# Kernel tuning notes

Hardware: AMD Instinct MI355X
Metric: run time of the kernel (lower is better)

## Reference

```python
import jax, jax.numpy as jnp
import numpy as np

NEG_INF = -1e30

def dwconv1(x, dw, db, pw, pb):
    # DWConv with kernel_size=1: depthwise = per-channel scale+bias, pointwise = dense linear.
    # x: [B, L, H]
    return (x * dw + db) @ pw.T + pb

def masked_softmax(logits, maskf, axis):
    # masked_softmax as in SQuAD repos: mask*logits + (1-mask)*(-1e30), then softmax over axis
    m = maskf * logits + (1.0 - maskf) * NEG_INF
    return jax.nn.softmax(m, axis=axis)

def setup_inputs() -> dict:
    key = jax.random.key(0)
    ks = jax.random.split(key, 20)
    B, L, H = 4, 4096, 1024
    s = 1.0 / np.sqrt(H)
    inp = {
        "x": jax.random.normal(ks[0], (B, L, H), dtype=jnp.float32),
        "mask": jax.random.randint(ks[1], (B, L), 0, 2, dtype=jnp.int32),
    }
    names = ["k", "q", "v", "r"]
    for i, n in enumerate(names):
        inp[n + "_dw"] = jax.random.normal(ks[2 + 4 * i], (H,), dtype=jnp.float32) * 0.1 + 1.0
        inp[n + "_db"] = jnp.zeros((H,), dtype=jnp.float32)
        inp[n + "_pw"] = jax.random.normal(ks[3 + 4 * i], (H, H), dtype=jnp.float32) * s
        inp[n + "_pb"] = jnp.zeros((H,), dtype=jnp.float32)
    return inp

def reference(x, mask, k_dw, k_db, k_pw, k_pb, q_dw, q_db, q_pw, q_pb,
              v_dw, v_db, v_pw, v_pb, r_dw, r_db, r_pw, r_pb):
    B, L, H = x.shape
    n_head = 16
    hc = H // n_head
    maskf = mask.astype(x.dtype)[:, None, None, :]  # [B,1,1,L]

    def heads(t):  # [B,L,H] -> [B,nh,hc,L]
        return t.reshape(B, L, n_head, hc).transpose(0, 2, 3, 1)

    keys = heads(dwconv1(x, k_dw, k_db, k_pw, k_pb))
    queries = heads(dwconv1(x, q_dw, q_db, q_pw, q_pb))
    values = heads(dwconv1(x, v_dw, v_db, v_pw, v_pb))

    key_sm = masked_softmax(keys, maskf, axis=3)      # softmax over L
    query_sm = masked_softmax(queries, maskf, axis=2)  # softmax over head channels

    # context = key @ value^T : [B,nh,hc,hc]
    context = jnp.einsum("bhcl,bhdl->bhcd", key_sm, values)
    # attended = context^T @ query : [B,nh,hc(value),L]
    attended = jnp.einsum("bhcd,bhcl->bhdl", context, query_sm)

    agg = attended.transpose(0, 3, 1, 2).reshape(B, L, H)  # concat heads, [B,L,H]
    # dropout is identity in eval mode
    return dwconv1(agg, r_dw, r_db, r_pw, r_pb)
```

## Files before the change

### kernel.cpp

```cpp
#include <hip/hip_runtime.h>
#include <stdint.h>

#define H 1024
#define LSEQ 4096
#define NBATCH 4
#define MT (NBATCH*LSEQ)

typedef __attribute__((ext_vector_type(8))) short bf16x8;
typedef __attribute__((ext_vector_type(4))) short s16x4;
typedef __attribute__((ext_vector_type(4))) float f32x4;

static __device__ __forceinline__ unsigned short f2bf(float f){
  union { float f; unsigned u; } v; v.f = f;
  unsigned u = v.u;
  return (unsigned short)((u + 0x7FFFu + ((u >> 16) & 1u)) >> 16);
}
static __device__ __forceinline__ float bf2f(unsigned short h){
  union { unsigned u; float f; } v; v.u = ((unsigned)h) << 16;
  return v.f;
}
static __device__ __forceinline__ void g2l16(const void* g, void* l){
  __builtin_amdgcn_global_load_lds((const __attribute__((address_space(1))) void*)g,
                                   (__attribute__((address_space(3))) void*)l, 16, 0, 0);
}
static __device__ __forceinline__ f32x4 mfma16(bf16x8 a, bf16x8 b, f32x4 c){
  return __builtin_amdgcn_mfma_f32_16x16x32_bf16(a, b, c, 0, 0, 0);
}

struct P4 { const float* pw[4]; const float* dw[4]; const float* db[4]; const float* pb[4]; };

__global__ __launch_bounds__(256) void prep_w(P4 a, short* __restrict__ wb, float* __restrict__ bo){
  __shared__ float red[256];
  const int g = blockIdx.x, p = g >> 10, j = g & 1023, t = threadIdx.x;
  const float* row = a.pw[p] + (size_t)j * H;
  const float* dwp = a.dw[p];
  const float* dbp = a.db[p];
  float acc = 0.f;
  #pragma unroll
  for (int k = 0; k < 4; ++k){
    int i = k*256 + t;
    float pv = row[i];
    wb[((size_t)p*H + j)*H + i] = (short)f2bf(pv * dwp[i]);
    acc += dbp[i] * pv;
  }
  red[t] = acc; __syncthreads();
  for (int s = 128; s > 0; s >>= 1){
    if (t < s) red[t] += red[t+s];
    __syncthreads();
  }
  if (t == 0) bo[p*H + j] = a.pb[p][j] + red[0];
}

__global__ __launch_bounds__(256) void cvt_x(const float* __restrict__ x, short* __restrict__ xb){
  int i = blockIdx.x*256 + threadIdx.x;
  const float4* p = (const float4*)(x + (size_t)i*8);
  float4 a = p[0], b = p[1];
  bf16x8 o;
  o[0]=(short)f2bf(a.x); o[1]=(short)f2bf(a.y); o[2]=(short)f2bf(a.z); o[3]=(short)f2bf(a.w);
  o[4]=(short)f2bf(b.x); o[5]=(short)f2bf(b.y); o[6]=(short)f2bf(b.z); o[7]=(short)f2bf(b.w);
  *(bf16x8*)(xb + (size_t)i*8) = o;
}

template<int MODE, int NBLK>
__global__ __launch_bounds__(512, 2) void gemm8(const short* __restrict__ A,
    const short* __restrict__ WBp, const float* __restrict__ bia,
    short* __restrict__ oq, short* __restrict__ okT, short* __restrict__ ovT,
    float* __restrict__ ofin){
  __shared__ __align__(16) short lA[2][256*64];
  __shared__ __align__(16) short lB[2][256*64];

  const int nwg = NBLK * 64;
  const int cpx = nwg >> 3;
  const int bid = blockIdx.x;
  const int swz = (bid & 7) * cpx + (bid >> 3);
  const int mb = swz / NBLK, nb = swz % NBLK;
  const int m0 = mb * 256, n0 = nb * 256;

  const int tid  = threadIdx.x;
  const int lane = tid & 63;
  const int w    = tid >> 6;
  const int wm   = w >> 2, wn = w & 3;
  const int q4 = lane >> 4, r16 = lane & 15;
  const int rl = lane >> 3, sl = lane & 7;
  const int srcsw = ((sl ^ rl) << 3);

#define STAGE_A(BUF_, Q_, KB_) \
  g2l16(A + (size_t)(m0 + (Q_)*64 + w*8 + rl)*H + (KB_) + srcsw, \
        &lA[BUF_][((Q_)*64 + w*8)*64])
#define STAGE_B(BUF_, Q_, KB_) \
  g2l16(WBp + (size_t)(n0 + (Q_)*64 + w*8 + rl)*H + (KB_) + srcsw, \
        &lB[BUF_][((Q_)*64 + w*8)*64])
#define RD_A(dst, BUF_, MI8, KK) { const int row_ = wm*128 + (MI8)*16 + r16; \
  dst = *(const bf16x8*)&lA[BUF_][row_*64 + ((((KK)*4+q4) ^ (row_&7))<<3)]; }
#define RD_B(dst, BUF_, NI4, KK) { const int row_ = wn*64 + (NI4)*16 + r16; \
  dst = *(const bf16x8*)&lB[BUF_][row_*64 + ((((KK)*4+q4) ^ (row_&7))<<3)]; }

  f32x4 acc[8][4] = {};
  bf16x8 aF[4][2], bFa[2][2], bFb[2][2];

  STAGE_B(0,0,0); STAGE_B(0,1,0); STAGE_B(0,2,0); STAGE_B(0,3,0);
  STAGE_A(0,0,0); STAGE_A(0,2,0); STAGE_A(0,1,0); STAGE_A(0,3,0);
  asm volatile("s_waitcnt vmcnt(2)" ::: "memory");
  __builtin_amdgcn_s_barrier();
  __builtin_amdgcn_sched_barrier(0);

  #pragma unroll 2
  for (int t = 0; t < 16; ++t){
    const int buf = t & 1, sbuf = buf ^ 1;
    const int skb = ((t < 15) ? (t + 1) : 15) << 6;

    #pragma unroll
    for (int mi = 0; mi < 4; ++mi){ RD_A(aF[mi][0], buf, mi, 0); RD_A(aF[mi][1], buf, mi, 1); }
    #pragma unroll
    for (int ni = 0; ni < 2; ++ni){ RD_B(bFa[ni][0], buf, ni, 0); RD_B(bFa[ni][1], buf, ni, 1); }
    STAGE_B(sbuf, 0, skb); STAGE_B(sbuf, 1, skb);
    __builtin_amdgcn_s_barrier();
    asm volatile("s_waitcnt lgkmcnt(0)" ::: "memory");
    __builtin_amdgcn_sched_barrier(0);
    __builtin_amdgcn_s_setprio(1);
    #pragma unroll
    for (int kk = 0; kk < 2; ++kk)
      #pragma unroll
      for (int mi = 0; mi < 4; ++mi)
        #pragma unroll
        for (int ni = 0; ni < 2; ++ni)
          acc[mi][ni] = mfma16(aF[mi][kk], bFa[ni][kk], acc[mi][ni]);
    __builtin_amdgcn_s_setprio(0);
    __builtin_amdgcn_s_barrier();
    __builtin_amdgcn_sched_barrier(0);

    #pragma unroll
    for (int ni = 0; ni < 2; ++ni){ RD_B(bFb[ni][0], buf, 2+ni, 0); RD_B(bFb[ni][1], buf, 2+ni, 1); }
    STAGE_B(sbuf, 2, skb); STAGE_B(sbuf, 3, skb);
    __builtin_amdgcn_s_barrier();
    asm volatile("s_waitcnt lgkmcnt(0)" ::: "memory");
    __builtin_amdgcn_sched_barrier(0);
    __builtin_amdgcn_s_setprio(1);
    #pragma unroll
    for (int kk = 0; kk < 2; ++kk)
      #pragma unroll
      for (int mi = 0; mi < 4; ++mi)
        #pragma unroll
        for (int ni = 0; ni < 2; ++ni)
          acc[mi][2+ni] = mfma16(aF[mi][kk], bFb[ni][kk], acc[mi][2+ni]);
    __builtin_amdgcn_s_setprio(0);
    asm volatile("s_waitcnt vmcnt(4)" ::: "memory");
    __builtin_amdgcn_s_barrier();
    __builtin_amdgcn_sched_barrier(0);

    #pragma unroll
    for (int mi = 0; mi < 4; ++mi){ RD_A(aF[mi][0], buf, 4+mi, 0); RD_A(aF[mi][1], buf, 4+mi, 1); }
    STAGE_A(sbuf, 0, skb); STAGE_A(sbuf, 2, skb);
    __builtin_amdgcn_s_barrier();
    asm volatile("s_waitcnt lgkmcnt(0)" ::: "memory");
    __builtin_amdgcn_sched_barrier(0);
    __builtin_amdgcn_s_setprio(1);
    #pragma unroll
    for (int kk = 0; kk < 2; ++kk)
      #pragma unroll
      for (int mi = 0; mi < 4; ++mi)
        #pragma unroll
        for (int ni = 0; ni < 2; ++ni)
          acc[4+mi][ni] = mfma16(aF[mi][kk], bFa[ni][kk], acc[4+mi][ni]);
    __builtin_amdgcn_s_setprio(0);
    __builtin_amdgcn_s_barrier();
    __builtin_amdgcn_sched_barrier(0);

    STAGE_A(sbuf, 1, skb); STAGE_A(sbuf, 3, skb);
    __builtin_amdgcn_s_barrier();
    asm volatile("s_waitcnt lgkmcnt(0)" ::: "memory");
    __builtin_amdgcn_sched_barrier(0);
    __builtin_amdgcn_s_setprio(1);
    #pragma unroll
    for (int kk = 0; kk < 2; ++kk)
      #pragma unroll
      for (int mi = 0; mi < 4; ++mi)
        #pragma unroll
        for (int ni = 0; ni < 2; ++ni)
          acc[4+mi][2+ni] = mfma16(aF[mi][kk], bFb[ni][kk], acc[4+mi][2+ni]);
    __builtin_amdgcn_s_setprio(0);
    asm volatile("s_waitcnt vmcnt(2)" ::: "memory");
    __builtin_amdgcn_s_barrier();
    __builtin_amdgcn_sched_barrier(0);
  }
#undef STAGE_A
#undef STAGE_B
#undef RD_A
#undef RD_B

  if (MODE == 1){
    #pragma unroll
    for (int ni4 = 0; ni4 < 4; ++ni4){
      const int n = n0 + wn*64 + ni4*16 + r16;
      const float bv = bia[n];
      #pragma unroll
      for (int mi8 = 0; mi8 < 8; ++mi8){
        const int mbse = m0 + wm*128 + mi8*16 + q4*4;
        #pragma unroll
        for (int j = 0; j < 4; ++j)
          ofin[(size_t)(mbse+j)*H + n] = acc[mi8][ni4][j] + bv;
      }
    }
  } else {
    const int p = n0 >> 10;
    if (p == 1){
      #pragma unroll
      for (int ni4 = 0; ni4 < 4; ++ni4){
        const int n = n0 + wn*64 + ni4*16 + r16;
        const float bv = bia[n];
        const int ch = n & 1023;
        #pragma unroll
        for (int mi8 = 0; mi8 < 8; ++mi8){
          const int mbse = m0 + wm*128 + mi8*16 + q4*4;
          #pragma unroll
          for (int j = 0; j < 4; ++j)
            oq[(size_t)(mbse+j)*H + ch] = (short)f2bf(acc[mi8][ni4][j] + bv);
        }
      }
    } else {
      short* ot = (p == 0) ? okT : ovT;
      #pragma unroll
      for (int ni4 = 0; ni4 < 4; ++ni4){
        const int n = n0 + wn*64 + ni4*16 + r16;
        const float bv = bia[n];
        const int ch = n & 1023;
        #pragma unroll
        for (int mi8 = 0; mi8 < 8; ++mi8){
          const int m = m0 + wm*128 + mi8*16 + q4*4;
          const int bb = m >> 12, lpos = m & 4095;
          s16x4 v;
          #pragma unroll
          for (int j = 0; j < 4; ++j) v[j] = (short)f2bf(acc[mi8][ni4][j] + bv);
          *(s16x4*)&ot[((size_t)bb*H + ch)*LSEQ + lpos] = v;
        }
      }
    }
  }
}

__global__ __launch_bounds__(256) void key_stats(const short* __restrict__ kT,
    const int* __restrict__ mask, float* __restrict__ mx, float* __restrict__ rd){
  const int w = threadIdx.x >> 6, lane = threadIdx.x & 63;
  const int ch = blockIdx.x*4 + w;
  const int b = ch >> 10;
  const short* row = kT + (size_t)ch * LSEQ;
  const int* mrow = mask + (size_t)b * LSEQ;
  float vals[64];
  float m = -3e38f;
  #pragma unroll
  for (int it = 0; it < 8; ++it){
    const int l = it*512 + lane*8;
    bf16x8 v = *(const bf16x8*)&row[l];
    int4 k0 = *(const int4*)&mrow[l];
    int4 k1 = *(const int4*)&mrow[l+4];
    int mk[8] = {k0.x,k0.y,k0.z,k0.w,k1.x,k1.y,k1.z,k1.w};
    #pragma unroll
    for (int e=0;e<8;++e){
      float lg = mk[e] ? bf2f((unsigned short)v[e]) : -1e30f;
      vals[it*8+e] = lg;
      m = fmaxf(m, lg);
    }
  }
  #pragma unroll
  for (int off=32; off>=1; off>>=1) m = fmaxf(m, __shfl_xor(m, off));
  float s = 0.f;
  #pragma unroll
  for (int i=0;i<64;++i) s += __expf(vals[i]-m);
  #pragma unroll
  for (int off=32; off>=1; off>>=1) s += __shfl_xor(s, off);
  if (lane == 0){ mx[ch] = m; rd[ch] = 1.0f / s; }
}

__global__ __launch_bounds__(256) void ctx_k(const short* __restrict__ kT,
    const short* __restrict__ vT, const int* __restrict__ mask,
    const float* __restrict__ mx, const float* __restrict__ rd,
    float* __restrict__ ctxP){
  const int lc = blockIdx.x, h = blockIdx.y, b = blockIdx.z;
  __shared__ __align__(16) short lK[64*64];
  __shared__ __align__(16) short lV[64*64];
  __shared__ float sMx[64], sRd[64];
  __shared__ int sMk[64];
  const int tid = threadIdx.x, lane = tid & 63, w = tid >> 6;
  if (tid < 64){
    const int ch = b*1024 + h*64 + tid;
    sMx[tid] = mx[ch]; sRd[tid] = rd[ch];
  }
  f32x4 acc[4] = {};
  const short* kb = kT + (size_t)(b*16 + h)*64*LSEQ;
  const short* vb = vT + (size_t)(b*16 + h)*64*LSEQ;
  const int l0 = lc*1024;
  const int sl = lane & 7, rl = lane >> 3;
  const int lsw = ((sl ^ rl) << 3);
  for (int kc = 0; kc < 16; ++kc){
    __syncthreads();
    const int lb = l0 + kc*64;
    #pragma unroll
    for (int c = 0; c < 2; ++c){
      const int r = (w*2+c)*8 + rl;
      g2l16(kb + (size_t)r*LSEQ + lb + lsw, &lK[(w*2+c)*512]);
      g2l16(vb + (size_t)r*LSEQ + lb + lsw, &lV[(w*2+c)*512]);
    }
    if (tid < 64) sMk[tid] = mask[(size_t)b*LSEQ + lb + tid];
    __syncthreads();
    {
      const int row = lane;
      const float mxr = sMx[row], rdr = sRd[row];
      #pragma unroll
      for (int k2 = 0; k2 < 2; ++k2){
        const int slog = w*2 + k2;
        const int sp = slog ^ (row & 7);
        bf16x8 v = *(bf16x8*)&lK[row*64 + (sp<<3)];
        bf16x8 o;
        #pragma unroll
        for (int e=0;e<8;++e){
          const float f = bf2f((unsigned short)v[e]);
          const float lg = sMk[slog*8+e] ? f : -1e30f;
          o[e] = (short)f2bf(__expf(lg - mxr) * rdr);
        }
        *(bf16x8*)&lK[row*64 + (sp<<3)] = o;
      }
    }
    __syncthreads();
    const int q4 = lane >> 4, r16 = lane & 15;
    #pragma unroll
    for (int kk = 0; kk < 2; ++kk){
      const int slog = kk*4 + q4;
      const int rowA = w*16 + r16;
      bf16x8 a = *(bf16x8*)&lK[rowA*64 + ((slog ^ (rowA & 7))<<3)];
      #pragma unroll
      for (int ni = 0; ni < 4; ++ni){
        const int rowB = ni*16 + r16;
        bf16x8 bv = *(bf16x8*)&lV[rowB*64 + ((slog ^ (rowB & 7))<<3)];
        acc[ni] = mfma16(a, bv, acc[ni]);
      }
    }
  }
  const int q4 = lane >> 4, r16 = lane & 15;
  float* op = ctxP + (((size_t)(b*16 + h)*4 + lc) << 12);
  #pragma unroll
  for (int ni=0;ni<4;++ni){
    const int d = ni*16 + r16;
    #pragma unroll
    for (int j=0;j<4;++j){
      const int c = w*16 + q4*4 + j;
      op[c*64 + d] = acc[ni][j];
    }
  }
}

__global__ __launch_bounds__(256) void attd_k(const short* __restrict__ qb,
    const float* __restrict__ ctxP, const int* __restrict__ mask,
    short* __restrict__ agg){
  const int lcb = blockIdx.x, h = blockIdx.y, b = blockIdx.z;
  __shared__ __align__(16) short lQ[64*64];
  __shared__ __align__(16) short lCt[64*64];
  const int tid = threadIdx.x, lane = tid & 63, w = tid >> 6;
  {
    const int d = lane, g = w;
    const float* base = ctxP + ((size_t)(b*16 + h)*4 << 12);
    #pragma unroll
    for (int i=0;i<16;++i){
      const int c = g*16 + i;
      const float s = base[c*64+d] + base[4096+c*64+d] + base[8192+c*64+d] + base[12288+c*64+d];
      lCt[d*64 + ((((c>>3) ^ (d&7))<<3) | (c&7))] = (short)f2bf(s);
    }
  }
  const int l0g = b*LSEQ + lcb*1024;
  const int sl = lane & 7, rl = lane >> 3;
  const int lsw = ((sl ^ rl) << 3);
  for (int sc = 0; sc < 16; ++sc){
    __syncthreads();
    #pragma unroll
    for (int c = 0; c < 2; ++c){
      const int r = (w*2+c)*8 + rl;
      g2l16(qb + (size_t)(l0g + sc*64 + r)*H + h*64 + lsw, &lQ[(w*2+c)*512]);
    }
    __syncthreads();
    {
      const int row = w*16 + (lane & 15);
      const int q4 = lane >> 4;
      const int mk = mask[(size_t)b*LSEQ + lcb*1024 + sc*64 + row];
      float vals[16];
      float mxv = -3e38f;
      #pragma unroll
      for (int k2=0;k2<2;++k2){
        const int slog = q4*2 + k2;
        const int sp = slog ^ (row & 7);
        bf16x8 v = *(bf16x8*)&lQ[row*64 + (sp<<3)];
        #pragma unroll
        for (int e=0;e<8;++e){
          const float f = bf2f((unsigned short)v[e]);
          vals[k2*8+e] = f;
          mxv = fmaxf(mxv, f);
        }
      }
      mxv = fmaxf(mxv, __shfl_xor(mxv, 16));
      mxv = fmaxf(mxv, __shfl_xor(mxv, 32));
      float s = 0.f;
      #pragma unroll
      for (int e=0;e<16;++e){ vals[e] = __expf(vals[e]-mxv); s += vals[e]; }
      s += __shfl_xor(s, 16);
      s += __shfl_xor(s, 32);
      const float inv = 1.0f / s;
      #pragma unroll
      for (int k2=0;k2<2;++k2){
        const int slog = q4*2 + k2;
        const int sp = slog ^ (row & 7);
        bf16x8 o;
        #pragma unroll
        for (int e=0;e<8;++e)
          o[e] = (short)f2bf(mk ? vals[k2*8+e]*inv : 0.015625f);
        *(bf16x8*)&lQ[row*64 + (sp<<3)] = o;
      }
    }
    __syncthreads();
    f32x4 acc[4] = {};
    const int q4 = lane >> 4, r16 = lane & 15;
    #pragma unroll
    for (int kk=0;kk<2;++kk){
      const int slog = kk*4 + q4;
      const int rowA = w*16 + r16;
      bf16x8 a = *(bf16x8*)&lQ[rowA*64 + ((slog ^ (rowA&7))<<3)];
      #pragma unroll
      for (int ni=0;ni<4;++ni){
        const int rowB = ni*16 + r16;
        bf16x8 bv = *(bf16x8*)&lCt[rowB*64 + ((slog ^ (rowB&7))<<3)];
        acc[ni] = mfma16(a, bv, acc[ni]);
      }
    }
    #pragma unroll
    for (int ni=0;ni<4;++ni){
      const int d = ni*16 + r16;
      #pragma unroll
      for (int j=0;j<4;++j){
        const int lrow = w*16 + q4*4 + j;
        agg[(size_t)(l0g + sc*64 + lrow)*H + h*64 + d] = (short)f2bf(acc[ni][j]);
      }
    }
  }
}

extern "C" void kernel_launch(void* const* d_in, const int* in_sizes, int n_in,
                              void* d_out, int out_size, void* d_ws, size_t ws_size,
                              hipStream_t stream){
  (void)in_sizes; (void)n_in; (void)out_size; (void)ws_size;
  const float* x    = (const float*)d_in[0];
  const int*   mask = (const int*)d_in[1];
  P4 prm;
  for (int p2 = 0; p2 < 4; ++p2){
    prm.dw[p2] = (const float*)d_in[2 + 4*p2];
    prm.db[p2] = (const float*)d_in[3 + 4*p2];
    prm.pw[p2] = (const float*)d_in[4 + 4*p2];
    prm.pb[p2] = (const float*)d_in[5 + 4*p2];
  }
  char* ws = (char*)d_ws;
  short* WB   = (short*)(ws);
  float* BIAS = (float*)(ws + ((size_t)8<<20));
  float* MX   = BIAS + 4096;
  float* RD   = MX + 4096;
  short* XB   = (short*)(ws + ((size_t)9<<20));
  short* QB   = (short*)(ws + ((size_t)41<<20));
  short* KT   = (short*)(ws + ((size_t)73<<20));
  short* VT   = (short*)(ws + ((size_t)105<<20));
  float* CTXP = (float*)(ws + ((size_t)137<<20));
  short* AGG  = XB;

  prep_w<<<4096, 256, 0, stream>>>(prm, WB, BIAS);
  cvt_x<<<8192, 256, 0, stream>>>(x, XB);
  gemm8<0,12><<<768, 512, 0, stream>>>(XB, WB, BIAS, QB, KT, VT, nullptr);
  key_stats<<<1024, 256, 0, stream>>>(KT, mask, MX, RD);
  ctx_k<<<dim3(4,16,4), 256, 0, stream>>>(KT, VT, mask, MX, RD, CTXP);
  attd_k<<<dim3(4,16,4), 256, 0, stream>>>(QB, CTXP, mask, AGG);
  gemm8<1,4><<<256, 512, 0, stream>>>(AGG, WB + (size_t)3*H*H, BIAS + 3*1024,
                                      nullptr, nullptr, nullptr, (float*)d_out);
}
```

Baseline: 239.6 us.

## Merge GEMM MFMA phases and stage transposed K/V epilogue through LDS

Loads all four B fragments up front and merges each pair of MFMA phases into one, cutting the number of barriers per K iteration from eight to four. The transposed K/V epilogue now writes bf16 results into a swizzled LDS tile and reads them back as 16-byte rows, so global stores along L are fully coalesced instead of scattered 8-byte writes. A single LDS array replaces the separate A/B buffers so the epilogue can reuse it. This adds register pressure from holding more B fragments, plus two extra syncs in the epilogue.

```diff
diff --git a/kernel.cpp b/kernel.cpp
--- a/kernel.cpp
+++ b/kernel.cpp
@@ -66,8 +66,7 @@
     const short* __restrict__ WBp, const float* __restrict__ bia,
     short* __restrict__ oq, short* __restrict__ okT, short* __restrict__ ovT,
     float* __restrict__ ofin){
-  __shared__ __align__(16) short lA[2][256*64];
-  __shared__ __align__(16) short lB[2][256*64];
+  __shared__ __align__(16) short lsm[2][2][256*64];
 
   const int nwg = NBLK * 64;
   const int cpx = nwg >> 3;
@@ -86,14 +85,14 @@
 
 #define STAGE_A(BUF_, Q_, KB_) \
   g2l16(A + (size_t)(m0 + (Q_)*64 + w*8 + rl)*H + (KB_) + srcsw, \
-        &lA[BUF_][((Q_)*64 + w*8)*64])
+        &lsm[0][BUF_][((Q_)*64 + w*8)*64])
 #define STAGE_B(BUF_, Q_, KB_) \
   g2l16(WBp + (size_t)(n0 + (Q_)*64 + w*8 + rl)*H + (KB_) + srcsw, \
-        &lB[BUF_][((Q_)*64 + w*8)*64])
+        &lsm[1][BUF_][((Q_)*64 + w*8)*64])
 #define RD_A(dst, BUF_, MI8, KK) { const int row_ = wm*128 + (MI8)*16 + r16; \
-  dst = *(const bf16x8*)&lA[BUF_][row_*64 + ((((KK)*4+q4) ^ (row_&7))<<3)]; }
+  dst = *(const bf16x8*)&lsm[0][BUF_][row_*64 + ((((KK)*4+q4) ^ (row_&7))<<3)]; }
 #define RD_B(dst, BUF_, NI4, KK) { const int row_ = wn*64 + (NI4)*16 + r16; \
-  dst = *(const bf16x8*)&lB[BUF_][row_*64 + ((((KK)*4+q4) ^ (row_&7))<<3)]; }
+  dst = *(const bf16x8*)&lsm[1][BUF_][row_*64 + ((((KK)*4+q4) ^ (row_&7))<<3)]; }
 
   f32x4 acc[8][4] = {};
   bf16x8 aF[4][2], bFa[2][2], bFb[2][2];
@@ -113,24 +112,9 @@
     for (int mi = 0; mi < 4; ++mi){ RD_A(aF[mi][0], buf, mi, 0); RD_A(aF[mi][1], buf, mi, 1); }
     #pragma unroll
     for (int ni = 0; ni < 2; ++ni){ RD_B(bFa[ni][0], buf, ni, 0); RD_B(bFa[ni][1], buf, ni, 1); }
+    #pragma unroll
+    for (int ni = 0; ni < 2; ++ni){ RD_B(bFb[ni][0], buf, 2+ni, 0); RD_B(bFb[ni][1], buf, 2+ni, 1); }
     STAGE_B(sbuf, 0, skb); STAGE_B(sbuf, 1, skb);
-    __builtin_amdgcn_s_barrier();
-    asm volatile("s_waitcnt lgkmcnt(0)" ::: "memory");
-    __builtin_amdgcn_sched_barrier(0);
-    __builtin_amdgcn_s_setprio(1);
-    #pragma unroll
-    for (int kk = 0; kk < 2; ++kk)
-      #pragma unroll
-      for (int mi = 0; mi < 4; ++mi)
-        #pragma unroll
-        for (int ni = 0; ni < 2; ++ni)
-          acc[mi][ni] = mfma16(aF[mi][kk], bFa[ni][kk], acc[mi][ni]);
-    __builtin_amdgcn_s_setprio(0);
-    __builtin_amdgcn_s_barrier();
-    __builtin_amdgcn_sched_barrier(0);
-
-    #pragma unroll
-    for (int ni = 0; ni < 2; ++ni){ RD_B(bFb[ni][0], buf, 2+ni, 0); RD_B(bFb[ni][1], buf, 2+ni, 1); }
     STAGE_B(sbuf, 2, skb); STAGE_B(sbuf, 3, skb);
     __builtin_amdgcn_s_barrier();
     asm volatile("s_waitcnt lgkmcnt(0)" ::: "memory");
@@ -139,10 +123,14 @@
     #pragma unroll
     for (int kk = 0; kk < 2; ++kk)
       #pragma unroll
-      for (int mi = 0; mi < 4; ++mi)
+      for (int mi = 0; mi < 4; ++mi){
+        #pragma unroll
+        for (int ni = 0; ni < 2; ++ni)
+          acc[mi][ni] = mfma16(aF[mi][kk], bFa[ni][kk], acc[mi][ni]);
         #pragma unroll
         for (int ni = 0; ni < 2; ++ni)
           acc[mi][2+ni] = mfma16(aF[mi][kk], bFb[ni][kk], acc[mi][2+ni]);
+      }
     __builtin_amdgcn_s_setprio(0);
     asm volatile("s_waitcnt vmcnt(4)" ::: "memory");
     __builtin_amdgcn_s_barrier();
@@ -151,21 +139,6 @@
     #pragma unroll
     for (int mi = 0; mi < 4; ++mi){ RD_A(aF[mi][0], buf, 4+mi, 0); RD_A(aF[mi][1], buf, 4+mi, 1); }
     STAGE_A(sbuf, 0, skb); STAGE_A(sbuf, 2, skb);
-    __builtin_amdgcn_s_barrier();
-    asm volatile("s_waitcnt lgkmcnt(0)" ::: "memory");
-    __builtin_amdgcn_sched_barrier(0);
-    __builtin_amdgcn_s_setprio(1);
-    #pragma unroll
-    for (int kk = 0; kk < 2; ++kk)
-      #pragma unroll
-      for (int mi = 0; mi < 4; ++mi)
-        #pragma unroll
-        for (int ni = 0; ni < 2; ++ni)
-          acc[4+mi][ni] = mfma16(aF[mi][kk], bFa[ni][kk], acc[4+mi][ni]);
-    __builtin_amdgcn_s_setprio(0);
-    __builtin_amdgcn_s_barrier();
-    __builtin_amdgcn_sched_barrier(0);
-
     STAGE_A(sbuf, 1, skb); STAGE_A(sbuf, 3, skb);
     __builtin_amdgcn_s_barrier();
     asm volatile("s_waitcnt lgkmcnt(0)" ::: "memory");
@@ -174,10 +147,14 @@
     #pragma unroll
     for (int kk = 0; kk < 2; ++kk)
       #pragma unroll
-      for (int mi = 0; mi < 4; ++mi)
+      for (int mi = 0; mi < 4; ++mi){
+        #pragma unroll
+        for (int ni = 0; ni < 2; ++ni)
+          acc[4+mi][ni] = mfma16(aF[mi][kk], bFa[ni][kk], acc[4+mi][ni]);
         #pragma unroll
         for (int ni = 0; ni < 2; ++ni)
           acc[4+mi][2+ni] = mfma16(aF[mi][kk], bFb[ni][kk], acc[4+mi][2+ni]);
+      }
     __builtin_amdgcn_s_setprio(0);
     asm volatile("s_waitcnt vmcnt(2)" ::: "memory");
     __builtin_amdgcn_s_barrier();
@@ -218,21 +195,31 @@
         }
       }
     } else {
-      short* ot = (p == 0) ? okT : ovT;
+      asm volatile("s_waitcnt vmcnt(0)" ::: "memory");
+      __syncthreads();
+      char* sC = (char*)&lsm[0][0][0];
       #pragma unroll
       for (int ni4 = 0; ni4 < 4; ++ni4){
-        const int n = n0 + wn*64 + ni4*16 + r16;
-        const float bv = bia[n];
-        const int ch = n & 1023;
+        const int cr = wn*64 + ni4*16 + r16;
+        const float bv = bia[n0 + cr];
         #pragma unroll
         for (int mi8 = 0; mi8 < 8; ++mi8){
-          const int m = m0 + wm*128 + mi8*16 + q4*4;
-          const int bb = m >> 12, lpos = m & 4095;
+          const int s8 = wm*32 + mi8*4 + q4;
           s16x4 v;
           #pragma unroll
           for (int j = 0; j < 4; ++j) v[j] = (short)f2bf(acc[mi8][ni4][j] + bv);
-          *(s16x4*)&ot[((size_t)bb*H + ch)*LSEQ + lpos] = v;
+          *(s16x4*)(sC + cr*512 + ((s8 ^ ((cr & 7) << 1)) << 3)) = v;
         }
+      }
+      __syncthreads();
+      short* ot = (p == 0) ? okT : ovT;
+      const int ch0 = n0 & 1023, bb = m0 >> 12, lp0 = m0 & 4095;
+      const int c = lane & 31;
+      #pragma unroll
+      for (int it = 0; it < 16; ++it){
+        const int cr = it*16 + w*2 + (lane >> 5);
+        bf16x8 vv = *(bf16x8*)(sC + cr*512 + ((c ^ (cr & 7)) << 4));
+        *(bf16x8*)&ot[((size_t)bb*H + ch0 + cr)*LSEQ + lp0 + c*8] = vv;
       }
     }
   }
```

After: 227.8 us. 4.9% less time.
